# Performance work log

Hardware: AMD Instinct MI355X
Metric: run time of the kernel (lower is better)

Reference implementation:

```python
import jax, jax.numpy as jnp
import numpy as np

N = 50000      # nodes
E = 800000     # edges (before self-loops)
IN = 128       # in_channels
HID = 32       # hidden_channels
HEADS = 4
OUT = 2        # out_channels
NEG_SLOPE = 0.2  # PyG GATConv default LeakyReLU slope


def gat_layer(x, src, dst, W, a_src, a_dst, b, n_nodes, concat):
    """PyG GATConv (eval mode, self-loops already appended to src/dst).
    x: [N, in], W: [in, H*F], a_src/a_dst: [H, F], b: [H*F] or [F].
    """
    H, F = a_src.shape
    h = (x @ W).reshape(n_nodes, H, F)              # [N, H, F]
    al_s = (h * a_src).sum(-1)                      # [N, H] per-node src logit
    al_d = (h * a_dst).sum(-1)                      # [N, H] per-node dst logit
    e = al_s[src] + al_d[dst]                       # [E', H]
    e = jnp.where(e > 0, e, NEG_SLOPE * e)          # LeakyReLU
    # segment softmax over edges grouped by destination node
    m = jax.ops.segment_max(e, dst, num_segments=n_nodes)
    m = jnp.where(jnp.isfinite(m), m, 0.0)
    num = jnp.exp(e - m[dst])                       # [E', H]
    den = jax.ops.segment_sum(num, dst, num_segments=n_nodes)
    alpha = num / (den[dst] + 1e-16)                # [E', H]
    out = jax.ops.segment_sum(alpha[:, :, None] * h[src], dst, num_segments=n_nodes)  # [N, H, F]
    out = out.reshape(n_nodes, H * F) if concat else out.mean(axis=1)
    return out + b


def setup_inputs() -> dict:
    key = jax.random.key(0)
    ks = jax.random.split(key, 16)
    HID4 = HID // 4
    inp = {
        "x": jax.random.normal(ks[0], (N, IN), dtype=jnp.float32),
        "edge_index": jax.random.randint(ks[1], (2, E), 0, N, dtype=jnp.int64),
        "edge_attr": jax.random.normal(ks[2], (E, 8), dtype=jnp.float32),
        # conv1: in=IN -> HID per head, HEADS heads, concat
        "W1": jax.random.normal(ks[3], (IN, HEADS * HID), dtype=jnp.float32) * (1.0 / np.sqrt(IN)),
        "a_src1": jax.random.normal(ks[4], (HEADS, HID), dtype=jnp.float32) * 0.1,
        "a_dst1": jax.random.normal(ks[5], (HEADS, HID), dtype=jnp.float32) * 0.1,
        "b1": jnp.zeros((HEADS * HID,), dtype=jnp.float32),
        # conv2: in=HEADS*HID -> HID//4, 1 head, mean (concat=False)
        "W2": jax.random.normal(ks[6], (HEADS * HID, HID4), dtype=jnp.float32) * (1.0 / np.sqrt(HEADS * HID)),
        "a_src2": jax.random.normal(ks[7], (1, HID4), dtype=jnp.float32) * 0.1,
        "a_dst2": jax.random.normal(ks[8], (1, HID4), dtype=jnp.float32) * 0.1,
        "b2": jnp.zeros((HID4,), dtype=jnp.float32),
        # final linear
        "Wl": jax.random.normal(ks[9], (HID4, OUT), dtype=jnp.float32) * (1.0 / np.sqrt(HID4)),
        "bl": jnp.zeros((OUT,), dtype=jnp.float32),
    }
    return inp


def reference(x, edge_index, edge_attr, W1, a_src1, a_dst1, b1,
              W2, a_src2, a_dst2, b2, Wl, bl):
    # edge_attr is ignored (GATConv built without edge_dim). Eval mode: dropout is identity.
    loop = jnp.arange(N, dtype=edge_index.dtype)
    src = jnp.concatenate([edge_index[0], loop])  # PyG adds self-loops by default
    dst = jnp.concatenate([edge_index[1], loop])
    h = jax.nn.elu(gat_layer(x, src, dst, W1, a_src1, a_dst1, b1, N, concat=True))
    h = jax.nn.elu(gat_layer(h, src, dst, W2, a_src2, a_dst2, b2, N, concat=False))
    return jax.nn.sigmoid(h @ Wl + bl)
```

## Files before the change

### kernel.cpp

```cpp
#include <hip/hip_runtime.h>
#include <math.h>

#define TPB 256
#define GN 64
#define CAP 64
#define NPASS 2
#define LOG2E 1.44269504088896f

typedef short bf16x8 __attribute__((ext_vector_type(8)));
typedef float floatx4 __attribute__((ext_vector_type(4)));
typedef int   intx4  __attribute__((ext_vector_type(4)));

__device__ __forceinline__ float elu_f(float x)  { return x > 0.f ? x : __expf(x) - 1.f; }
__device__ __forceinline__ float sigmoid_f(float x){ return 1.f / (1.f + __expf(-x)); }
__device__ __forceinline__ float leaky(float x)  { return fmaxf(x, 0.2f * x); }

__device__ __forceinline__ unsigned short f2bf(float f) {
    unsigned int u = __float_as_uint(f);
    return (unsigned short)((u + 0x7FFFu + ((u >> 16) & 1u)) >> 16);
}
__device__ __forceinline__ float bf_lo(unsigned int u) { return __uint_as_float(u << 16); }
__device__ __forceinline__ float bf_hi(unsigned int u) { return __uint_as_float(u & 0xffff0000u); }

static inline int cdiv(long long a, int b) { return (int)((a + b - 1) / b); }

__global__ void init_wt(int* __restrict__ cursor, unsigned short* __restrict__ slots,
                        const float* __restrict__ W, unsigned short* __restrict__ wtg,
                        int IB, int N) {
    if (blockIdx.x < (unsigned)IB) {
        int i = blockIdx.x * blockDim.x + threadIdx.x;
        if (i < N) {
            cursor[i] = 1;
            slots[(size_t)i << 6] = (unsigned short)i;
        }
        return;
    }
    int idx = (blockIdx.x - IB) * blockDim.x + threadIdx.x;
    int k = idx >> 5;
    int c4 = (idx & 31) * 4;
    float4 v = *(const float4*)(W + (size_t)k * 128 + c4);
    wtg[(size_t)(c4 + 0) * 128 + k] = f2bf(v.x);
    wtg[(size_t)(c4 + 1) * 128 + k] = f2bf(v.y);
    wtg[(size_t)(c4 + 2) * 128 + k] = f2bf(v.z);
    wtg[(size_t)(c4 + 3) * 128 + k] = f2bf(v.w);
}

__global__ __launch_bounds__(256) void scatter_gemm(
        const float* __restrict__ x, const unsigned short* __restrict__ wtg,
        const float* __restrict__ a_src, const float* __restrict__ a_dst,
        unsigned short* __restrict__ hb, float* __restrict__ als, float* __restrict__ ald,
        const int* __restrict__ ei, int E, float invg,
        int* __restrict__ cursor, unsigned short* __restrict__ slots,
        int SB, int PPB, int GBn, int N) {
    __shared__ unsigned short xs[GN][136];
    int tid = threadIdx.x;

    int TOT = SB + GBn;
    long long bi = blockIdx.x;
    int gprev = (int)((bi * (long long)GBn) / TOT);
    bool isg = (int)(((bi + 1) * (long long)GBn) / TOT) > gprev;

    if (!isg) {
        int sb = blockIdx.x - gprev;
        int p = sb / PPB;
        int eb = sb - p * PPB;
        int base = (eb * TPB + tid) * 4;
        if (base >= E) return;
        int d[4], s[4];
        bool ok[4];
        if (base + 3 < E) {
            intx4 dv = __builtin_nontemporal_load((const intx4*)(ei + E + base));
            intx4 sv = __builtin_nontemporal_load((const intx4*)(ei + base));
            d[0] = dv.x; d[1] = dv.y; d[2] = dv.z; d[3] = dv.w;
            s[0] = sv.x; s[1] = sv.y; s[2] = sv.z; s[3] = sv.w;
#pragma unroll
            for (int j = 0; j < 4; j++)
                ok[j] = ((int)((float)d[j] * invg) == p);
        } else {
#pragma unroll
            for (int j = 0; j < 4; j++) {
                int e = base + j;
                bool in = e < E;
                d[j] = in ? ei[E + e] : 0;
                s[j] = in ? ei[e] : 0;
                ok[j] = in && ((int)((float)d[j] * invg) == p);
            }
        }
#pragma unroll
        for (int j = 0; j < 4; j++) {
            if (ok[j]) {
                int pos = atomicAdd(&cursor[d[j]], 1);
                if (pos < CAP) slots[((size_t)d[j] << 6) + pos] = (unsigned short)s[j];
            }
        }
        return;
    }

    int n0 = gprev * GN;
#pragma unroll
    for (int i = 0; i < 8; i++) {
        int idx = tid + i * 256;
        int r = idx >> 5;
        int c4 = (idx & 31) * 4;
        int row = n0 + r; if (row >= N) row = N - 1;
        floatx4 v = __builtin_nontemporal_load((const floatx4*)(x + (size_t)row * 128 + c4));
        unsigned short* pp = &xs[r][c4];
        pp[0] = f2bf(v[0]); pp[1] = f2bf(v[1]); pp[2] = f2bf(v[2]); pp[3] = f2bf(v[3]);
    }
    __syncthreads();

    int w = tid >> 6;
    int lane = tid & 63;
    int idx16 = lane & 15, quad = lane >> 4;
    int nw = n0 + w * 16;

    bf16x8 af[4];
#pragma unroll
    for (int kc = 0; kc < 4; kc++)
        af[kc] = *(const bf16x8*)(&xs[w * 16 + idx16][kc * 32 + quad * 8]);

    floatx4 accs[8];
#pragma unroll
    for (int cg = 0; cg < 8; cg++) {
        floatx4 acc = {0.f, 0.f, 0.f, 0.f};
        const unsigned short* wrow = wtg + (size_t)(cg * 16 + idx16) * 128 + quad * 8;
#pragma unroll
        for (int kc = 0; kc < 4; kc++) {
            bf16x8 bf = *(const bf16x8*)(wrow + kc * 32);
            acc = __builtin_amdgcn_mfma_f32_16x16x32_bf16(af[kc], bf, acc, 0, 0, 0);
        }
        accs[cg] = acc;
    }

    float asr[8], adr[8];
#pragma unroll
    for (int cg = 0; cg < 8; cg++) {
        asr[cg] = a_src[cg * 16 + idx16];
        adr[cg] = a_dst[cg * 16 + idx16];
    }
    float ps[16], pd[16];
#pragma unroll
    for (int i = 0; i < 16; i++) { ps[i] = 0.f; pd[i] = 0.f; }
#pragma unroll
    for (int cg = 0; cg < 8; cg++) {
        int h = cg >> 1;
#pragma unroll
        for (int r = 0; r < 4; r++) {
            ps[r * 4 + h] = fmaf(accs[cg][r], asr[cg], ps[r * 4 + h]);
            pd[r * 4 + h] = fmaf(accs[cg][r], adr[cg], pd[r * 4 + h]);
        }
    }
#pragma unroll
    for (int i = 0; i < 16; i++) {
        ps[i] += __shfl_xor(ps[i], 1); ps[i] += __shfl_xor(ps[i], 2);
        ps[i] += __shfl_xor(ps[i], 4); ps[i] += __shfl_xor(ps[i], 8);
        pd[i] += __shfl_xor(pd[i], 1); pd[i] += __shfl_xor(pd[i], 2);
        pd[i] += __shfl_xor(pd[i], 4); pd[i] += __shfl_xor(pd[i], 8);
    }
    float myps = 0.f, mypd = 0.f;
#pragma unroll
    for (int i = 0; i < 16; i++) {
        if (i == idx16) { myps = ps[i]; mypd = pd[i]; }
    }
    int rowl = nw + quad * 4 + (idx16 >> 2);
    if (rowl < N) {
        als[rowl * 4 + (idx16 & 3)] = myps * LOG2E;
        ald[rowl * 4 + (idx16 & 3)] = mypd * LOG2E;
    }
#pragma unroll
    for (int cg = 0; cg < 8; cg++) {
#pragma unroll
        for (int r = 0; r < 4; r++) {
            int row = nw + quad * 4 + r;
            if (row < N)
                __builtin_nontemporal_store(f2bf(accs[cg][r]),
                                            &hb[(size_t)row * 128 + cg * 16 + idx16]);
        }
    }
}

__global__ void accum1_fused(const int* __restrict__ cursor, const unsigned short* __restrict__ slots,
                             const unsigned short* __restrict__ hb,
                             const float* __restrict__ als, const float* __restrict__ ald,
                             const float* __restrict__ b, const float* __restrict__ W2,
                             const float* __restrict__ a_src2, const float* __restrict__ a_dst2,
                             float* __restrict__ h2, float* __restrict__ als2,
                             float* __restrict__ ald2, int N) {
    int t = blockIdx.x * blockDim.x + threadIdx.x;
    int n = t >> 6;
    if (n >= N) return;
    int lane = t & 63;
    int eslot = lane >> 4;
    int fg = lane & 15;
    int hd = fg >> 2;

    float ald_h = ald[n * 4 + hd];
    int cnt = cursor[n]; if (cnt > CAP) cnt = CAP;
    const unsigned short* cp = slots + ((size_t)n << 6);

    int i0 = eslot < cnt ? eslot : cnt - 1;
    int s_c = cp[i0];
    float al_c = als[s_c * 4 + hd];
    uint4 u_c = *(const uint4*)(hb + (size_t)s_c * 128 + fg * 8);
    int i1 = 4 + eslot < cnt ? 4 + eslot : cnt - 1;
    int s_n = cp[i1];
    float al_n = als[s_n * 4 + hd];
    uint4 u_n = *(const uint4*)(hb + (size_t)s_n * 128 + fg * 8);

    float acc[8];
#pragma unroll
    for (int k = 0; k < 8; k++) acc[k] = 0.f;
    float den = 0.f;

    for (int base = 0; base < cnt; base += 4) {
        int nxt = base + 8 + eslot;
        int ic = nxt < cnt ? nxt : cnt - 1;
        int s_nn = cp[ic];
        float al_nn = als[s_nn * 4 + hd];
        uint4 u_nn = *(const uint4*)(hb + (size_t)s_nn * 128 + fg * 8);

        float w = exp2f(leaky(al_c + ald_h));
        if (base + eslot >= cnt) w = 0.f;
        acc[0] = fmaf(w, bf_lo(u_c.x), acc[0]);
        acc[1] = fmaf(w, bf_hi(u_c.x), acc[1]);
        acc[2] = fmaf(w, bf_lo(u_c.y), acc[2]);
        acc[3] = fmaf(w, bf_hi(u_c.y), acc[3]);
        acc[4] = fmaf(w, bf_lo(u_c.z), acc[4]);
        acc[5] = fmaf(w, bf_hi(u_c.z), acc[5]);
        acc[6] = fmaf(w, bf_lo(u_c.w), acc[6]);
        acc[7] = fmaf(w, bf_hi(u_c.w), acc[7]);
        den += w;

        al_c = al_n; u_c = u_n;
        al_n = al_nn; u_n = u_nn;
    }

#pragma unroll
    for (int k = 0; k < 8; k++) {
        acc[k] += __shfl_xor(acc[k], 16);
        acc[k] += __shfl_xor(acc[k], 32);
    }
    den += __shfl_xor(den, 16);
    den += __shfl_xor(den, 32);

    float inv = 1.f / (den + 1e-16f);
    float bv[8];
    *(float4*)(bv)     = *(const float4*)(b + fg * 8);
    *(float4*)(bv + 4) = *(const float4*)(b + fg * 8 + 4);
    float o[8];
#pragma unroll
    for (int k = 0; k < 8; k++) o[k] = elu_f(acc[k] * inv + bv[k]);

    int srcl = lane >> 2;
    float tmp[8];
#pragma unroll
    for (int k = 0; k < 8; k++) tmp[k] = __shfl(o[k], srcl);
    int sel = lane & 3;
    float o0 = sel == 0 ? tmp[0] : sel == 1 ? tmp[2] : sel == 2 ? tmp[4] : tmp[6];
    float o1 = sel == 0 ? tmp[1] : sel == 1 ? tmp[3] : sel == 2 ? tmp[5] : tmp[7];

    float w2a[8], w2b[8];
#pragma unroll
    for (int c = 0; c < 8; c += 4) {
        *(float4*)(w2a + c) = *(const float4*)(W2 + (size_t)(2 * lane) * 8 + c);
        *(float4*)(w2b + c) = *(const float4*)(W2 + (size_t)(2 * lane + 1) * 8 + c);
    }
    float part[8];
#pragma unroll
    for (int c = 0; c < 8; c++)
        part[c] = fmaf(o0, w2a[c], o1 * w2b[c]);
#pragma unroll
    for (int c = 0; c < 8; c++) {
        part[c] += __shfl_xor(part[c], 1);
        part[c] += __shfl_xor(part[c], 2);
        part[c] += __shfl_xor(part[c], 4);
    }
    int ch = lane & 7;
    float v = part[0];
    v = ch == 1 ? part[1] : v;  v = ch == 2 ? part[2] : v;  v = ch == 3 ? part[3] : v;
    v = ch == 4 ? part[4] : v;  v = ch == 5 ? part[5] : v;  v = ch == 6 ? part[6] : v;
    v = ch == 7 ? part[7] : v;
    v += __shfl_xor(v, 8); v += __shfl_xor(v, 16); v += __shfl_xor(v, 32);
    if (lane < 8) h2[(size_t)n * 8 + lane] = v;
    float ps2 = v * a_src2[ch];
    float pd2 = v * a_dst2[ch];
    ps2 += __shfl_xor(ps2, 1); ps2 += __shfl_xor(ps2, 2); ps2 += __shfl_xor(ps2, 4);
    pd2 += __shfl_xor(pd2, 1); pd2 += __shfl_xor(pd2, 2); pd2 += __shfl_xor(pd2, 4);
    if (lane == 0) {
        als2[n] = ps2 * LOG2E;
        ald2[n] = pd2 * LOG2E;
    }
}

__global__ void accum2_final(const int* __restrict__ cursor, const unsigned short* __restrict__ slots,
                             const float* __restrict__ h2,
                             const float* __restrict__ als, const float* __restrict__ ald,
                             const float* __restrict__ b2, const float* __restrict__ Wl,
                             const float* __restrict__ bl, float* __restrict__ out, int N) {
    int t = blockIdx.x * blockDim.x + threadIdx.x;
    int n = t >> 6;
    if (n >= N) return;
    int lane = t & 63;
    int slot = lane >> 3;
    int c = lane & 7;

    float ald_n = ald[n];
    int cnt = cursor[n]; if (cnt > CAP) cnt = CAP;
    const unsigned short* cp = slots + ((size_t)n << 6);

    int i0 = slot < cnt ? slot : cnt - 1;
    int s_c = cp[i0];
    float al_c = als[s_c];
    float h_c = h2[(size_t)s_c * 8 + c];
    int i1 = 8 + slot < cnt ? 8 + slot : cnt - 1;
    int s_n = cp[i1];
    float al_n = als[s_n];
    float h_n = h2[(size_t)s_n * 8 + c];

    float den = 0.f, acc = 0.f;
    for (int base = 0; base < cnt; base += 8) {
        int nxt = base + 16 + slot;
        int ic = nxt < cnt ? nxt : cnt - 1;
        int s_nn = cp[ic];
        float al_nn = als[s_nn];
        float h_nn = h2[(size_t)s_nn * 8 + c];

        float w = exp2f(leaky(al_c + ald_n));
        if (base + slot >= cnt) w = 0.f;
        acc = fmaf(w, h_c, acc);
        den += w;

        al_c = al_n; h_c = h_n;
        al_n = al_nn; h_n = h_nn;
    }
    acc += __shfl_xor(acc, 8);  acc += __shfl_xor(acc, 16); acc += __shfl_xor(acc, 32);
    den += __shfl_xor(den, 8);  den += __shfl_xor(den, 16); den += __shfl_xor(den, 32);

    float inv = 1.f / (den + 1e-16f);
    float o = elu_f(acc * inv + b2[c]);
    float r0 = o * Wl[c * 2 + 0];
    float r1 = o * Wl[c * 2 + 1];
    r0 += __shfl_xor(r0, 1); r0 += __shfl_xor(r0, 2); r0 += __shfl_xor(r0, 4);
    r1 += __shfl_xor(r1, 1); r1 += __shfl_xor(r1, 2); r1 += __shfl_xor(r1, 4);
    if (lane == 0) {
        float2 r;
        r.x = sigmoid_f(r0 + bl[0]);
        r.y = sigmoid_f(r1 + bl[1]);
        *(float2*)(out + (size_t)n * 2) = r;
    }
}

extern "C" void kernel_launch(void* const* d_in, const int* in_sizes, int n_in,
                              void* d_out, int out_size, void* d_ws, size_t ws_size,
                              hipStream_t stream) {
    const float* x      = (const float*)d_in[0];
    const int*   ei     = (const int*)d_in[1];
    const float* W1     = (const float*)d_in[3];
    const float* a_src1 = (const float*)d_in[4];
    const float* a_dst1 = (const float*)d_in[5];
    const float* b1     = (const float*)d_in[6];
    const float* W2     = (const float*)d_in[7];
    const float* a_src2 = (const float*)d_in[8];
    const float* a_dst2 = (const float*)d_in[9];
    const float* b2     = (const float*)d_in[10];
    const float* Wl     = (const float*)d_in[11];
    const float* bl     = (const float*)d_in[12];
    float* out = (float*)d_out;

    const int N = in_sizes[0] / 128;
    const int E = in_sizes[1] / 2;
    const int gsz = cdiv(N, NPASS);
    const float invg = 1.f / (float)gsz;
    const int GB = cdiv(N, GN);
    const int PPB = cdiv(cdiv(E, 4), TPB);
    const int SB = NPASS * PPB;
    const int IB = cdiv(N, TPB);

    unsigned short* h1b = (unsigned short*)d_ws;
    float* als1 = (float*)d_ws + (size_t)N * 64;
    float* ald1 = als1 + (size_t)N * 4;
    float* h2   = ald1 + (size_t)N * 4;
    float* als2 = h2   + (size_t)N * 8;
    float* ald2 = als2 + (size_t)N;
    int* cursor = (int*)(ald2 + (size_t)N);
    unsigned short* slots = (unsigned short*)(cursor + N);
    unsigned short* wtg = slots + ((size_t)N << 6);
    (void)ws_size; (void)n_in; (void)out_size;

    init_wt<<<IB + 16, TPB, 0, stream>>>(cursor, slots, W1, wtg, IB, N);
    scatter_gemm<<<SB + GB, 256, 0, stream>>>(x, wtg, a_src1, a_dst1, h1b, als1, ald1,
                                              ei, E, invg, cursor, slots, SB, PPB, GB, N);
    accum1_fused<<<cdiv((long long)N * 64, TPB), TPB, 0, stream>>>(
        cursor, slots, h1b, als1, ald1, b1, W2, a_src2, a_dst2, h2, als2, ald2, N);
    accum2_final<<<cdiv((long long)N * 64, TPB), TPB, 0, stream>>>(
        cursor, slots, h2, als2, ald2, b2, Wl, bl, out, N);
}
```

Baseline: 223.4 us.

## Pack per-node cursor and slots into 128-byte records and interleave layer-2 data

Each node's atomic counter and neighbor slot list now share one 128-byte record, so the count and the first slots arrive in the same cache line. Capacity drops from 64 to 62 to make room for the counter. Layer-2 features and both attention logits are packed into one 16-float row per node, so each gathered neighbor needs one line instead of separate loads. Nontemporal stores for the layer-1 features become plain stores, which may keep them cached for the next kernel. The lower capacity truncates neighbor lists earlier on high-degree nodes, although with average degree around 17 this rarely applies.

```diff
diff --git a/kernel.cpp b/kernel.cpp
--- a/kernel.cpp
+++ b/kernel.cpp
@@ -3,7 +3,7 @@
 
 #define TPB 256
 #define GN 64
-#define CAP 64
+#define CAP 62
 #define NPASS 2
 #define LOG2E 1.44269504088896f
 
@@ -24,14 +24,15 @@
 
 static inline int cdiv(long long a, int b) { return (int)((a + b - 1) / b); }
 
-__global__ void init_wt(int* __restrict__ cursor, unsigned short* __restrict__ slots,
+__global__ void init_wt(char* __restrict__ rec,
                         const float* __restrict__ W, unsigned short* __restrict__ wtg,
                         int IB, int N) {
     if (blockIdx.x < (unsigned)IB) {
         int i = blockIdx.x * blockDim.x + threadIdx.x;
         if (i < N) {
-            cursor[i] = 1;
-            slots[(size_t)i << 6] = (unsigned short)i;
+            char* rp = rec + ((size_t)i << 7);
+            *(int*)rp = 1;
+            *(unsigned short*)(rp + 4) = (unsigned short)i;
         }
         return;
     }
@@ -50,7 +51,7 @@
         const float* __restrict__ a_src, const float* __restrict__ a_dst,
         unsigned short* __restrict__ hb, float* __restrict__ als, float* __restrict__ ald,
         const int* __restrict__ ei, int E, float invg,
-        int* __restrict__ cursor, unsigned short* __restrict__ slots,
+        char* __restrict__ rec,
         int SB, int PPB, int GBn, int N) {
     __shared__ unsigned short xs[GN][136];
     int tid = threadIdx.x;
@@ -89,8 +90,9 @@
 #pragma unroll
         for (int j = 0; j < 4; j++) {
             if (ok[j]) {
-                int pos = atomicAdd(&cursor[d[j]], 1);
-                if (pos < CAP) slots[((size_t)d[j] << 6) + pos] = (unsigned short)s[j];
+                char* rp = rec + ((size_t)d[j] << 7);
+                int pos = atomicAdd((int*)rp, 1);
+                if (pos < CAP) *(unsigned short*)(rp + 4 + 2 * pos) = (unsigned short)s[j];
             }
         }
         return;
@@ -172,20 +174,17 @@
 #pragma unroll
         for (int r = 0; r < 4; r++) {
             int row = nw + quad * 4 + r;
-            if (row < N)
-                __builtin_nontemporal_store(f2bf(accs[cg][r]),
-                                            &hb[(size_t)row * 128 + cg * 16 + idx16]);
-        }
-    }
-}
-
-__global__ void accum1_fused(const int* __restrict__ cursor, const unsigned short* __restrict__ slots,
+            if (row < N) hb[(size_t)row * 128 + cg * 16 + idx16] = f2bf(accs[cg][r]);
+        }
+    }
+}
+
+__global__ void accum1_fused(const char* __restrict__ rec,
                              const unsigned short* __restrict__ hb,
                              const float* __restrict__ als, const float* __restrict__ ald,
                              const float* __restrict__ b, const float* __restrict__ W2,
                              const float* __restrict__ a_src2, const float* __restrict__ a_dst2,
-                             float* __restrict__ h2, float* __restrict__ als2,
-                             float* __restrict__ ald2, int N) {
+                             float* __restrict__ h2x, int N) {
     int t = blockIdx.x * blockDim.x + threadIdx.x;
     int n = t >> 6;
     if (n >= N) return;
@@ -195,8 +194,9 @@
     int hd = fg >> 2;
 
     float ald_h = ald[n * 4 + hd];
-    int cnt = cursor[n]; if (cnt > CAP) cnt = CAP;
-    const unsigned short* cp = slots + ((size_t)n << 6);
+    const char* rp = rec + ((size_t)n << 7);
+    int cnt = *(const int*)rp; if (cnt > CAP) cnt = CAP;
+    const unsigned short* cp = (const unsigned short*)(rp + 4);
 
     int i0 = eslot < cnt ? eslot : cnt - 1;
     int s_c = cp[i0];
@@ -281,20 +281,18 @@
     v = ch == 4 ? part[4] : v;  v = ch == 5 ? part[5] : v;  v = ch == 6 ? part[6] : v;
     v = ch == 7 ? part[7] : v;
     v += __shfl_xor(v, 8); v += __shfl_xor(v, 16); v += __shfl_xor(v, 32);
-    if (lane < 8) h2[(size_t)n * 8 + lane] = v;
     float ps2 = v * a_src2[ch];
     float pd2 = v * a_dst2[ch];
     ps2 += __shfl_xor(ps2, 1); ps2 += __shfl_xor(ps2, 2); ps2 += __shfl_xor(ps2, 4);
     pd2 += __shfl_xor(pd2, 1); pd2 += __shfl_xor(pd2, 2); pd2 += __shfl_xor(pd2, 4);
-    if (lane == 0) {
-        als2[n] = ps2 * LOG2E;
-        ald2[n] = pd2 * LOG2E;
-    }
-}
-
-__global__ void accum2_final(const int* __restrict__ cursor, const unsigned short* __restrict__ slots,
-                             const float* __restrict__ h2,
-                             const float* __restrict__ als, const float* __restrict__ ald,
+    float outv = v;
+    if (lane == 8) outv = ps2 * LOG2E;
+    if (lane == 9) outv = pd2 * LOG2E;
+    if (lane < 10) h2x[(size_t)n * 16 + lane] = outv;
+}
+
+__global__ void accum2_final(const char* __restrict__ rec,
+                             const float* __restrict__ h2x,
                              const float* __restrict__ b2, const float* __restrict__ Wl,
                              const float* __restrict__ bl, float* __restrict__ out, int N) {
     int t = blockIdx.x * blockDim.x + threadIdx.x;
@@ -304,26 +302,27 @@
     int slot = lane >> 3;
     int c = lane & 7;
 
-    float ald_n = ald[n];
-    int cnt = cursor[n]; if (cnt > CAP) cnt = CAP;
-    const unsigned short* cp = slots + ((size_t)n << 6);
+    const char* rp = rec + ((size_t)n << 7);
+    int cnt = *(const int*)rp; if (cnt > CAP) cnt = CAP;
+    const unsigned short* cp = (const unsigned short*)(rp + 4);
+    float ald_n = h2x[(size_t)n * 16 + 9];
 
     int i0 = slot < cnt ? slot : cnt - 1;
     int s_c = cp[i0];
-    float al_c = als[s_c];
-    float h_c = h2[(size_t)s_c * 8 + c];
+    float al_c = h2x[(size_t)s_c * 16 + 8];
+    float h_c = h2x[(size_t)s_c * 16 + c];
     int i1 = 8 + slot < cnt ? 8 + slot : cnt - 1;
     int s_n = cp[i1];
-    float al_n = als[s_n];
-    float h_n = h2[(size_t)s_n * 8 + c];
+    float al_n = h2x[(size_t)s_n * 16 + 8];
+    float h_n = h2x[(size_t)s_n * 16 + c];
 
     float den = 0.f, acc = 0.f;
     for (int base = 0; base < cnt; base += 8) {
         int nxt = base + 16 + slot;
         int ic = nxt < cnt ? nxt : cnt - 1;
         int s_nn = cp[ic];
-        float al_nn = als[s_nn];
-        float h_nn = h2[(size_t)s_nn * 8 + c];
+        float al_nn = h2x[(size_t)s_nn * 16 + 8];
+        float h_nn = h2x[(size_t)s_nn * 16 + c];
 
         float w = exp2f(leaky(al_c + ald_n));
         if (base + slot >= cnt) w = 0.f;
@@ -379,19 +378,16 @@
     unsigned short* h1b = (unsigned short*)d_ws;
     float* als1 = (float*)d_ws + (size_t)N * 64;
     float* ald1 = als1 + (size_t)N * 4;
-    float* h2   = ald1 + (size_t)N * 4;
-    float* als2 = h2   + (size_t)N * 8;
-    float* ald2 = als2 + (size_t)N;
-    int* cursor = (int*)(ald2 + (size_t)N);
-    unsigned short* slots = (unsigned short*)(cursor + N);
-    unsigned short* wtg = slots + ((size_t)N << 6);
+    float* h2x  = ald1 + (size_t)N * 4;
+    char*  rec  = (char*)(h2x + (size_t)N * 16);
+    unsigned short* wtg = (unsigned short*)(rec + ((size_t)N << 7));
     (void)ws_size; (void)n_in; (void)out_size;
 
-    init_wt<<<IB + 16, TPB, 0, stream>>>(cursor, slots, W1, wtg, IB, N);
+    init_wt<<<IB + 16, TPB, 0, stream>>>(rec, W1, wtg, IB, N);
     scatter_gemm<<<SB + GB, 256, 0, stream>>>(x, wtg, a_src1, a_dst1, h1b, als1, ald1,
-                                              ei, E, invg, cursor, slots, SB, PPB, GB, N);
+                                              ei, E, invg, rec, SB, PPB, GB, N);
     accum1_fused<<<cdiv((long long)N * 64, TPB), TPB, 0, stream>>>(
-        cursor, slots, h1b, als1, ald1, b1, W2, a_src2, a_dst2, h2, als2, ald2, N);
+        rec, h1b, als1, ald1, b1, W2, a_src2, a_dst2, h2x, N);
     accum2_final<<<cdiv((long long)N * 64, TPB), TPB, 0, stream>>>(
-        cursor, slots, h2, als2, ald2, b2, Wl, bl, out, N);
-}
+        rec, h2x, b2, Wl, bl, out, N);
+}
```

New measurement: 237.5 us. +6.3%, slower.

## Widen per-lane gathers, pack layer-2 features with logits, drop nontemporal stores

Applied to the files above, without the earlier changes.

In the layer-1 aggregation, each lane now handles 16 features (two 16-byte loads) and 8 edges are processed per iteration instead of 4. The second-layer matmul is restructured so each lane multiplies its 16 outputs against W2 directly, with no cross-lane redistribution. Layer-2 features and their src/dst logits are packed into one 16-float row per node, so the final kernel gathers each neighbor's logit and features from a single cache line, handling 16 edges per iteration with float2 loads. The bf16 h1 stores become ordinary stores so the gathers that follow can hit in L2. The cost is more registers per thread and a padded 64-byte record per node.

```diff
diff --git a/kernel.cpp b/kernel.cpp
--- a/kernel.cpp
+++ b/kernel.cpp
@@ -172,9 +172,7 @@
 #pragma unroll
         for (int r = 0; r < 4; r++) {
             int row = nw + quad * 4 + r;
-            if (row < N)
-                __builtin_nontemporal_store(f2bf(accs[cg][r]),
-                                            &hb[(size_t)row * 128 + cg * 16 + idx16]);
+            if (row < N) hb[(size_t)row * 128 + cg * 16 + idx16] = f2bf(accs[cg][r]);
         }
     }
 }
@@ -184,15 +182,14 @@
                              const float* __restrict__ als, const float* __restrict__ ald,
                              const float* __restrict__ b, const float* __restrict__ W2,
                              const float* __restrict__ a_src2, const float* __restrict__ a_dst2,
-                             float* __restrict__ h2, float* __restrict__ als2,
-                             float* __restrict__ ald2, int N) {
+                             float* __restrict__ h2x, int N) {
     int t = blockIdx.x * blockDim.x + threadIdx.x;
     int n = t >> 6;
     if (n >= N) return;
     int lane = t & 63;
-    int eslot = lane >> 4;
-    int fg = lane & 15;
-    int hd = fg >> 2;
+    int eslot = lane >> 3;
+    int fg = lane & 7;
+    int hd = fg >> 1;
 
     float ald_h = ald[n * 4 + hd];
     int cnt = cursor[n]; if (cnt > CAP) cnt = CAP;
@@ -201,147 +198,165 @@
     int i0 = eslot < cnt ? eslot : cnt - 1;
     int s_c = cp[i0];
     float al_c = als[s_c * 4 + hd];
-    uint4 u_c = *(const uint4*)(hb + (size_t)s_c * 128 + fg * 8);
-    int i1 = 4 + eslot < cnt ? 4 + eslot : cnt - 1;
+    uint4 uc0 = *(const uint4*)(hb + (size_t)s_c * 128 + fg * 16);
+    uint4 uc1 = *(const uint4*)(hb + (size_t)s_c * 128 + fg * 16 + 8);
+    int i1 = 8 + eslot < cnt ? 8 + eslot : cnt - 1;
     int s_n = cp[i1];
     float al_n = als[s_n * 4 + hd];
-    uint4 u_n = *(const uint4*)(hb + (size_t)s_n * 128 + fg * 8);
-
-    float acc[8];
-#pragma unroll
-    for (int k = 0; k < 8; k++) acc[k] = 0.f;
+    uint4 un0 = *(const uint4*)(hb + (size_t)s_n * 128 + fg * 16);
+    uint4 un1 = *(const uint4*)(hb + (size_t)s_n * 128 + fg * 16 + 8);
+
+    float acc[16];
+#pragma unroll
+    for (int k = 0; k < 16; k++) acc[k] = 0.f;
     float den = 0.f;
 
-    for (int base = 0; base < cnt; base += 4) {
-        int nxt = base + 8 + eslot;
+    for (int base = 0; base < cnt; base += 8) {
+        int nxt = base + 16 + eslot;
         int ic = nxt < cnt ? nxt : cnt - 1;
         int s_nn = cp[ic];
         float al_nn = als[s_nn * 4 + hd];
-        uint4 u_nn = *(const uint4*)(hb + (size_t)s_nn * 128 + fg * 8);
+        uint4 unn0 = *(const uint4*)(hb + (size_t)s_nn * 128 + fg * 16);
+        uint4 unn1 = *(const uint4*)(hb + (size_t)s_nn * 128 + fg * 16 + 8);
 
         float w = exp2f(leaky(al_c + ald_h));
         if (base + eslot >= cnt) w = 0.f;
-        acc[0] = fmaf(w, bf_lo(u_c.x), acc[0]);
-        acc[1] = fmaf(w, bf_hi(u_c.x), acc[1]);
-        acc[2] = fmaf(w, bf_lo(u_c.y), acc[2]);
-        acc[3] = fmaf(w, bf_hi(u_c.y), acc[3]);
-        acc[4] = fmaf(w, bf_lo(u_c.z), acc[4]);
-        acc[5] = fmaf(w, bf_hi(u_c.z), acc[5]);
-        acc[6] = fmaf(w, bf_lo(u_c.w), acc[6]);
-        acc[7] = fmaf(w, bf_hi(u_c.w), acc[7]);
+        acc[0]  = fmaf(w, bf_lo(uc0.x), acc[0]);
+        acc[1]  = fmaf(w, bf_hi(uc0.x), acc[1]);
+        acc[2]  = fmaf(w, bf_lo(uc0.y), acc[2]);
+        acc[3]  = fmaf(w, bf_hi(uc0.y), acc[3]);
+        acc[4]  = fmaf(w, bf_lo(uc0.z), acc[4]);
+        acc[5]  = fmaf(w, bf_hi(uc0.z), acc[5]);
+        acc[6]  = fmaf(w, bf_lo(uc0.w), acc[6]);
+        acc[7]  = fmaf(w, bf_hi(uc0.w), acc[7]);
+        acc[8]  = fmaf(w, bf_lo(uc1.x), acc[8]);
+        acc[9]  = fmaf(w, bf_hi(uc1.x), acc[9]);
+        acc[10] = fmaf(w, bf_lo(uc1.y), acc[10]);
+        acc[11] = fmaf(w, bf_hi(uc1.y), acc[11]);
+        acc[12] = fmaf(w, bf_lo(uc1.z), acc[12]);
+        acc[13] = fmaf(w, bf_hi(uc1.z), acc[13]);
+        acc[14] = fmaf(w, bf_lo(uc1.w), acc[14]);
+        acc[15] = fmaf(w, bf_hi(uc1.w), acc[15]);
         den += w;
 
-        al_c = al_n; u_c = u_n;
-        al_n = al_nn; u_n = u_nn;
-    }
-
-#pragma unroll
-    for (int k = 0; k < 8; k++) {
+        al_c = al_n; uc0 = un0; uc1 = un1;
+        al_n = al_nn; un0 = unn0; un1 = unn1;
+    }
+
+#pragma unroll
+    for (int k = 0; k < 16; k++) {
+        acc[k] += __shfl_xor(acc[k], 8);
         acc[k] += __shfl_xor(acc[k], 16);
         acc[k] += __shfl_xor(acc[k], 32);
     }
+    den += __shfl_xor(den, 8);
     den += __shfl_xor(den, 16);
     den += __shfl_xor(den, 32);
 
     float inv = 1.f / (den + 1e-16f);
-    float bv[8];
-    *(float4*)(bv)     = *(const float4*)(b + fg * 8);
-    *(float4*)(bv + 4) = *(const float4*)(b + fg * 8 + 4);
-    float o[8];
-#pragma unroll
-    for (int k = 0; k < 8; k++) o[k] = elu_f(acc[k] * inv + bv[k]);
-
-    int srcl = lane >> 2;
-    float tmp[8];
-#pragma unroll
-    for (int k = 0; k < 8; k++) tmp[k] = __shfl(o[k], srcl);
-    int sel = lane & 3;
-    float o0 = sel == 0 ? tmp[0] : sel == 1 ? tmp[2] : sel == 2 ? tmp[4] : tmp[6];
-    float o1 = sel == 0 ? tmp[1] : sel == 1 ? tmp[3] : sel == 2 ? tmp[5] : tmp[7];
-
-    float w2a[8], w2b[8];
-#pragma unroll
-    for (int c = 0; c < 8; c += 4) {
-        *(float4*)(w2a + c) = *(const float4*)(W2 + (size_t)(2 * lane) * 8 + c);
-        *(float4*)(w2b + c) = *(const float4*)(W2 + (size_t)(2 * lane + 1) * 8 + c);
-    }
+    float bv[16];
+#pragma unroll
+    for (int k = 0; k < 16; k += 4)
+        *(float4*)(bv + k) = *(const float4*)(b + fg * 16 + k);
+    float o[16];
+#pragma unroll
+    for (int k = 0; k < 16; k++) o[k] = elu_f(acc[k] * inv + bv[k]);
+
     float part[8];
 #pragma unroll
-    for (int c = 0; c < 8; c++)
-        part[c] = fmaf(o0, w2a[c], o1 * w2b[c]);
+    for (int c = 0; c < 8; c++) part[c] = 0.f;
+#pragma unroll
+    for (int kk = 0; kk < 16; kk++) {
+        const float* wr = W2 + (size_t)(fg * 16 + kk) * 8;
+        float4 wa = *(const float4*)wr;
+        float4 wb = *(const float4*)(wr + 4);
+        part[0] = fmaf(o[kk], wa.x, part[0]);
+        part[1] = fmaf(o[kk], wa.y, part[1]);
+        part[2] = fmaf(o[kk], wa.z, part[2]);
+        part[3] = fmaf(o[kk], wa.w, part[3]);
+        part[4] = fmaf(o[kk], wb.x, part[4]);
+        part[5] = fmaf(o[kk], wb.y, part[5]);
+        part[6] = fmaf(o[kk], wb.z, part[6]);
+        part[7] = fmaf(o[kk], wb.w, part[7]);
+    }
 #pragma unroll
     for (int c = 0; c < 8; c++) {
         part[c] += __shfl_xor(part[c], 1);
         part[c] += __shfl_xor(part[c], 2);
         part[c] += __shfl_xor(part[c], 4);
+    }
+    float ps2 = 0.f, pd2 = 0.f;
+#pragma unroll
+    for (int c = 0; c < 8; c++) {
+        ps2 = fmaf(part[c], a_src2[c], ps2);
+        pd2 = fmaf(part[c], a_dst2[c], pd2);
     }
     int ch = lane & 7;
     float v = part[0];
     v = ch == 1 ? part[1] : v;  v = ch == 2 ? part[2] : v;  v = ch == 3 ? part[3] : v;
     v = ch == 4 ? part[4] : v;  v = ch == 5 ? part[5] : v;  v = ch == 6 ? part[6] : v;
     v = ch == 7 ? part[7] : v;
-    v += __shfl_xor(v, 8); v += __shfl_xor(v, 16); v += __shfl_xor(v, 32);
-    if (lane < 8) h2[(size_t)n * 8 + lane] = v;
-    float ps2 = v * a_src2[ch];
-    float pd2 = v * a_dst2[ch];
-    ps2 += __shfl_xor(ps2, 1); ps2 += __shfl_xor(ps2, 2); ps2 += __shfl_xor(ps2, 4);
-    pd2 += __shfl_xor(pd2, 1); pd2 += __shfl_xor(pd2, 2); pd2 += __shfl_xor(pd2, 4);
-    if (lane == 0) {
-        als2[n] = ps2 * LOG2E;
-        ald2[n] = pd2 * LOG2E;
-    }
+    float outv = v;
+    if (lane == 8) outv = ps2 * LOG2E;
+    if (lane == 9) outv = pd2 * LOG2E;
+    if (lane < 10) h2x[(size_t)n * 16 + lane] = outv;
 }
 
 __global__ void accum2_final(const int* __restrict__ cursor, const unsigned short* __restrict__ slots,
-                             const float* __restrict__ h2,
-                             const float* __restrict__ als, const float* __restrict__ ald,
+                             const float* __restrict__ h2x,
                              const float* __restrict__ b2, const float* __restrict__ Wl,
                              const float* __restrict__ bl, float* __restrict__ out, int N) {
     int t = blockIdx.x * blockDim.x + threadIdx.x;
     int n = t >> 6;
     if (n >= N) return;
     int lane = t & 63;
-    int slot = lane >> 3;
-    int c = lane & 7;
-
-    float ald_n = ald[n];
+    int slot = lane >> 2;
+    int cpair = (lane & 3) * 2;
+
     int cnt = cursor[n]; if (cnt > CAP) cnt = CAP;
     const unsigned short* cp = slots + ((size_t)n << 6);
+    float ald_n = h2x[(size_t)n * 16 + 9];
 
     int i0 = slot < cnt ? slot : cnt - 1;
     int s_c = cp[i0];
-    float al_c = als[s_c];
-    float h_c = h2[(size_t)s_c * 8 + c];
-    int i1 = 8 + slot < cnt ? 8 + slot : cnt - 1;
+    float al_c = h2x[(size_t)s_c * 16 + 8];
+    float2 h_c = *(const float2*)(h2x + (size_t)s_c * 16 + cpair);
+    int i1 = 16 + slot < cnt ? 16 + slot : cnt - 1;
     int s_n = cp[i1];
-    float al_n = als[s_n];
-    float h_n = h2[(size_t)s_n * 8 + c];
-
-    float den = 0.f, acc = 0.f;
-    for (int base = 0; base < cnt; base += 8) {
-        int nxt = base + 16 + slot;
+    float al_n = h2x[(size_t)s_n * 16 + 8];
+    float2 h_n = *(const float2*)(h2x + (size_t)s_n * 16 + cpair);
+
+    float den = 0.f, acc0 = 0.f, acc1 = 0.f;
+    for (int base = 0; base < cnt; base += 16) {
+        int nxt = base + 32 + slot;
         int ic = nxt < cnt ? nxt : cnt - 1;
         int s_nn = cp[ic];
-        float al_nn = als[s_nn];
-        float h_nn = h2[(size_t)s_nn * 8 + c];
+        float al_nn = h2x[(size_t)s_nn * 16 + 8];
+        float2 h_nn = *(const float2*)(h2x + (size_t)s_nn * 16 + cpair);
 
         float w = exp2f(leaky(al_c + ald_n));
         if (base + slot >= cnt) w = 0.f;
-        acc = fmaf(w, h_c, acc);
+        acc0 = fmaf(w, h_c.x, acc0);
+        acc1 = fmaf(w, h_c.y, acc1);
         den += w;
 
         al_c = al_n; h_c = h_n;
         al_n = al_nn; h_n = h_nn;
     }
-    acc += __shfl_xor(acc, 8);  acc += __shfl_xor(acc, 16); acc += __shfl_xor(acc, 32);
-    den += __shfl_xor(den, 8);  den += __shfl_xor(den, 16); den += __shfl_xor(den, 32);
+    acc0 += __shfl_xor(acc0, 4);  acc0 += __shfl_xor(acc0, 8);
+    acc0 += __shfl_xor(acc0, 16); acc0 += __shfl_xor(acc0, 32);
+    acc1 += __shfl_xor(acc1, 4);  acc1 += __shfl_xor(acc1, 8);
+    acc1 += __shfl_xor(acc1, 16); acc1 += __shfl_xor(acc1, 32);
+    den  += __shfl_xor(den, 4);   den  += __shfl_xor(den, 8);
+    den  += __shfl_xor(den, 16);  den  += __shfl_xor(den, 32);
 
     float inv = 1.f / (den + 1e-16f);
-    float o = elu_f(acc * inv + b2[c]);
-    float r0 = o * Wl[c * 2 + 0];
-    float r1 = o * Wl[c * 2 + 1];
-    r0 += __shfl_xor(r0, 1); r0 += __shfl_xor(r0, 2); r0 += __shfl_xor(r0, 4);
-    r1 += __shfl_xor(r1, 1); r1 += __shfl_xor(r1, 2); r1 += __shfl_xor(r1, 4);
+    float o0 = elu_f(acc0 * inv + b2[cpair]);
+    float o1 = elu_f(acc1 * inv + b2[cpair + 1]);
+    float r0 = o0 * Wl[cpair * 2 + 0] + o1 * Wl[(cpair + 1) * 2 + 0];
+    float r1 = o0 * Wl[cpair * 2 + 1] + o1 * Wl[(cpair + 1) * 2 + 1];
+    r0 += __shfl_xor(r0, 1); r0 += __shfl_xor(r0, 2);
+    r1 += __shfl_xor(r1, 1); r1 += __shfl_xor(r1, 2);
     if (lane == 0) {
         float2 r;
         r.x = sigmoid_f(r0 + bl[0]);
@@ -379,10 +394,8 @@
     unsigned short* h1b = (unsigned short*)d_ws;
     float* als1 = (float*)d_ws + (size_t)N * 64;
     float* ald1 = als1 + (size_t)N * 4;
-    float* h2   = ald1 + (size_t)N * 4;
-    float* als2 = h2   + (size_t)N * 8;
-    float* ald2 = als2 + (size_t)N;
-    int* cursor = (int*)(ald2 + (size_t)N);
+    float* h2x  = ald1 + (size_t)N * 4;
+    int* cursor = (int*)(h2x + (size_t)N * 16);
     unsigned short* slots = (unsigned short*)(cursor + N);
     unsigned short* wtg = slots + ((size_t)N << 6);
     (void)ws_size; (void)n_in; (void)out_size;
@@ -391,7 +404,7 @@
     scatter_gemm<<<SB + GB, 256, 0, stream>>>(x, wtg, a_src1, a_dst1, h1b, als1, ald1,
                                               ei, E, invg, cursor, slots, SB, PPB, GB, N);
     accum1_fused<<<cdiv((long long)N * 64, TPB), TPB, 0, stream>>>(
-        cursor, slots, h1b, als1, ald1, b1, W2, a_src2, a_dst2, h2, als2, ald2, N);
+        cursor, slots, h1b, als1, ald1, b1, W2, a_src2, a_dst2, h2x, N);
     accum2_final<<<cdiv((long long)N * 64, TPB), TPB, 0, stream>>>(
-        cursor, slots, h2, als2, ald2, b2, Wl, bl, out, N);
-}
+        cursor, slots, h2x, b2, Wl, bl, out, N);
+}
```

Result: slower. 374.5 us (+67.6%).
